# Kernel tuning notes

Hardware: AMD Instinct MI355X
Metric: run time of the kernel (lower is better)

The kernel has to match this reference:

```python
import jax, jax.numpy as jnp
import numpy as np

N, M, D = 8192, 8192, 256

def setup_inputs() -> dict:
    key = jax.random.key(0)
    k1, k2, k3, k4 = jax.random.split(key, 4)
    x1 = jax.random.normal(k1, (N, D), dtype=jnp.float32)
    x2 = jax.random.normal(k2, (M, D), dtype=jnp.float32)
    alpha_raw = jax.random.normal(k3, (D,), dtype=jnp.float32)      # nn.Parameter(torch.randn(input_dim))
    variance_raw = jnp.ones((1,), dtype=jnp.float32)                # nn.Parameter(torch.ones(1))
    return {"x1": x1, "x2": x2, "alpha_raw": alpha_raw, "variance_raw": variance_raw}

def reference(x1, x2, alpha_raw, variance_raw):
    # alpha = softmax(alpha_raw^2), variance = variance_raw^2
    alpha = jax.nn.softmax(alpha_raw ** 2)                          # (D,)
    variance = variance_raw ** 2                                    # (1,)
    # GEMM rewrite of sum_d alpha_d (x1_i - x2_j)^2:
    #   ||x1*sqrt(a)||^2 - 2 (x1*sqrt(a))(x2*sqrt(a))^T + ||x2*sqrt(a)||^2
    sa = jnp.sqrt(alpha)
    a = x1 * sa                                                     # (N, D)
    b = x2 * sa                                                     # (M, D)
    sq = (jnp.sum(a * a, axis=-1)[:, None]
          - 2.0 * (a @ b.T)
          + jnp.sum(b * b, axis=-1)[None, :])                       # (N, M)
    sq = jnp.maximum(sq, 0.0)  # numerical guard; exact value is non-negative
    kernel = variance * jnp.exp(-0.5 * sq)                          # (N, M)
    if kernel.shape[0] == 1:
        kernel = jnp.squeeze(kernel)
    return kernel
```

## Files before the change

### kernel.cpp

```cpp
#include <hip/hip_runtime.h>
#include <stdint.h>

#define NROWS 8192
#define MCOLS 8192
#define KDIM  256

typedef __bf16 bf16x8 __attribute__((ext_vector_type(8)));
typedef float  floatx4 __attribute__((ext_vector_type(4)));
typedef unsigned short ushort4v __attribute__((ext_vector_type(4)));

__device__ __forceinline__ unsigned short f32_to_bf16_rne(float f) {
    unsigned int u = __float_as_uint(f);
    u += 0x7FFFu + ((u >> 16) & 1u);
    return (unsigned short)(u >> 16);
}
__device__ __forceinline__ float bf16_to_f32(unsigned short h) {
    return __uint_as_float(((unsigned int)h) << 16);
}

__device__ __forceinline__ void async16(const void* g, void* l) {
    __builtin_amdgcn_global_load_lds(
        (const __attribute__((address_space(1))) unsigned int*)g,
        (__attribute__((address_space(3))) unsigned int*)l,
        16, 0, 0);
}

__global__ void prep_alpha(const float* __restrict__ araw, float* __restrict__ sa) {
    int d = threadIdx.x;
    float z = araw[d];
    z = z * z;
    float m = z;
#pragma unroll
    for (int off = 32; off; off >>= 1) m = fmaxf(m, __shfl_xor(m, off));
    __shared__ float wred[4];
    if ((d & 63) == 0) wred[d >> 6] = m;
    __syncthreads();
    float mx = fmaxf(fmaxf(wred[0], wred[1]), fmaxf(wred[2], wred[3]));
    float e = __expf(z - mx);
    float s = e;
#pragma unroll
    for (int off = 32; off; off >>= 1) s += __shfl_xor(s, off);
    __syncthreads();
    if ((d & 63) == 0) wred[d >> 6] = s;
    __syncthreads();
    float sum = wred[0] + wred[1] + wred[2] + wred[3];
    sa[d] = sqrtf(e / sum);
}

__global__ void prep_rows(const float* __restrict__ x1, const float* __restrict__ x2,
                          const float* __restrict__ sa,
                          unsigned short* __restrict__ Amat, unsigned short* __restrict__ Bmat,
                          float* __restrict__ ra, float* __restrict__ rb) {
    int wave = threadIdx.x >> 6;
    int lane = threadIdx.x & 63;
    int grow = blockIdx.x * 4 + wave;
    const float* x; unsigned short* mat; float* nrm; int row;
    if (grow < NROWS) { x = x1; mat = Amat; nrm = ra; row = grow; }
    else              { x = x2; mat = Bmat; nrm = rb; row = grow - NROWS; }

    floatx4 v  = *(const floatx4*)&x[(size_t)row * KDIM + lane * 4];
    floatx4 sv = *(const floatx4*)&sa[lane * 4];
    ushort4v h;
    float p = 0.0f;
#pragma unroll
    for (int j = 0; j < 4; ++j) {
        float f = v[j] * sv[j];
        unsigned short hh = f32_to_bf16_rne(f);
        h[j] = hh;
        float fv = bf16_to_f32(hh);
        p += fv * fv;
    }
    *(ushort4v*)&mat[(size_t)row * KDIM + lane * 4] = h;
#pragma unroll
    for (int off = 32; off; off >>= 1) p += __shfl_xor(p, off);
    if (lane == 0) nrm[row] = p;
}

__global__ __launch_bounds__(256) void rbf_gemm(
    const unsigned short* __restrict__ A, const unsigned short* __restrict__ B,
    const float* __restrict__ ra, const float* __restrict__ rb,
    const float* __restrict__ vraw, float* __restrict__ out)
{
    __shared__ unsigned short As[128 * 64];
    __shared__ unsigned short Bs[128 * 64];

    const int tid  = threadIdx.x;
    const int lane = tid & 63;
    const int wave = tid >> 6;

    const int g   = blockIdx.y * gridDim.x + blockIdx.x;
    const int xcd = g & 7;
    const int i   = g >> 3;
    const int bm  = (xcd >> 2) * 32 + (i >> 4);
    const int bn  = (xcd & 3) * 16 + (i & 15);

    const int wm = (wave & 1) * 64;
    const int wn = (wave >> 1) * 64;
    const int quad = lane >> 4;
    const int l15  = lane & 15;

    floatx4 acc[4][4];
#pragma unroll
    for (int tj = 0; tj < 4; tj++)
#pragma unroll
        for (int ti = 0; ti < 4; ti++) acc[tj][ti] = (floatx4)0.0f;

    for (int t = 0; t < 4; ++t) {
        int k0 = t * 64;
#pragma unroll
        for (int it = 0; it < 4; ++it) {
            int c   = it * 256 + tid;
            int row = c >> 3;
            int kc  = c & 7;
            int gkc = kc ^ (row & 7);
            const unsigned short* gA = A + (size_t)(bm * 128 + row) * KDIM + k0 + gkc * 8;
            const unsigned short* gB = B + (size_t)(bn * 128 + row) * KDIM + k0 + gkc * 8;
            async16(gA, &As[c * 8]);
            async16(gB, &Bs[c * 8]);
        }
        __syncthreads();

#pragma unroll
        for (int ks = 0; ks < 2; ++ks) {
            bf16x8 af[4], bfr[4];
            int kc = ks * 4 + quad;
#pragma unroll
            for (int tt = 0; tt < 4; ++tt) {
                int m   = wm + tt * 16 + l15;
                int sA  = m * 8 + (kc ^ (m & 7));
                af[tt]  = *(const bf16x8*)&As[sA * 8];
                int n   = wn + tt * 16 + l15;
                int sB  = n * 8 + (kc ^ (n & 7));
                bfr[tt] = *(const bf16x8*)&Bs[sB * 8];
            }
#pragma unroll
            for (int tj = 0; tj < 4; ++tj)
#pragma unroll
                for (int ti = 0; ti < 4; ++ti)
                    acc[tj][ti] = __builtin_amdgcn_mfma_f32_16x16x32_bf16(
                        bfr[tj], af[ti], acc[tj][ti], 0, 0, 0);
        }
        if (t < 3) __syncthreads();
    }

    float variance = vraw[0] * vraw[0];
#pragma unroll
    for (int ti = 0; ti < 4; ++ti) {
        int row = bm * 128 + wm + ti * 16 + l15;
        float rav = ra[row];
        float* orow = out + (size_t)row * MCOLS;
#pragma unroll
        for (int tj = 0; tj < 4; ++tj) {
            int nbase = bn * 128 + wn + tj * 16 + quad * 4;
            floatx4 rbv = *(const floatx4*)&rb[nbase];
            floatx4 val;
#pragma unroll
            for (int r = 0; r < 4; ++r) {
                float s = rav + rbv[r] - 2.0f * acc[tj][ti][r];
                s = fmaxf(s, 0.0f);
                val[r] = variance * __expf(-0.5f * s);
            }
            *(floatx4*)&orow[nbase] = val;
        }
    }
}

extern "C" void kernel_launch(void* const* d_in, const int* in_sizes, int n_in,
                              void* d_out, int out_size, void* d_ws, size_t ws_size,
                              hipStream_t stream) {
    const float* x1   = (const float*)d_in[0];
    const float* x2   = (const float*)d_in[1];
    const float* araw = (const float*)d_in[2];
    const float* vraw = (const float*)d_in[3];
    float* out = (float*)d_out;

    char* ws = (char*)d_ws;
    float* sa = (float*)ws;
    float* ra = (float*)(ws + 1024);
    float* rb = (float*)(ws + 1024 + 32768);
    unsigned short* Amat = (unsigned short*)(ws + 66560);
    unsigned short* Bmat = (unsigned short*)(ws + 66560 + (size_t)NROWS * KDIM * 2);

    prep_alpha<<<1, 256, 0, stream>>>(araw, sa);
    prep_rows<<<(NROWS + MCOLS) / 4, 256, 0, stream>>>(x1, x2, sa, Amat, Bmat, ra, rb);

    dim3 grid(MCOLS / 128, NROWS / 128);
    rbf_gemm<<<grid, 256, 0, stream>>>(Amat, Bmat, ra, rb, vraw, out);
}
```

Baseline: 304.6 us.

## Fuse alpha softmax into row prep and process two tiles per GEMM block

Each prep_rows block now computes the softmax of alpha itself into LDS, which removes the separate single-block prep_alpha launch and its global round trip. The GEMM kernel now launches 2048 blocks that each handle two output tiles. It issues the first k-slice load of the second tile before the first tile's epilogue so that load overlaps the exp/store work. Launch bounds request 4 blocks per CU. The trade-off is redundant softmax work in every prep block and fewer total blocks.

Result: slower. 339.5 us (+11.5%).

```diff
diff --git a/kernel.cpp b/kernel.cpp
--- a/kernel.cpp
+++ b/kernel.cpp
@@ -25,41 +25,41 @@
         16, 0, 0);
 }
 
-__global__ void prep_alpha(const float* __restrict__ araw, float* __restrict__ sa) {
-    int d = threadIdx.x;
-    float z = araw[d];
+__global__ void prep_rows(const float* __restrict__ x1, const float* __restrict__ x2,
+                          const float* __restrict__ araw,
+                          unsigned short* __restrict__ Amat, unsigned short* __restrict__ Bmat,
+                          float* __restrict__ ra, float* __restrict__ rb) {
+    __shared__ float sa_lds[256];
+    __shared__ float wred[8];
+    int tid  = threadIdx.x;
+    int wave = tid >> 6;
+    int lane = tid & 63;
+
+    float z = araw[tid];
     z = z * z;
     float m = z;
 #pragma unroll
     for (int off = 32; off; off >>= 1) m = fmaxf(m, __shfl_xor(m, off));
-    __shared__ float wred[4];
-    if ((d & 63) == 0) wred[d >> 6] = m;
+    if (lane == 0) wred[wave] = m;
     __syncthreads();
     float mx = fmaxf(fmaxf(wred[0], wred[1]), fmaxf(wred[2], wred[3]));
     float e = __expf(z - mx);
     float s = e;
 #pragma unroll
     for (int off = 32; off; off >>= 1) s += __shfl_xor(s, off);
+    if (lane == 0) wred[4 + wave] = s;
     __syncthreads();
-    if ((d & 63) == 0) wred[d >> 6] = s;
+    float sum = wred[4] + wred[5] + wred[6] + wred[7];
+    sa_lds[tid] = sqrtf(e / sum);
     __syncthreads();
-    float sum = wred[0] + wred[1] + wred[2] + wred[3];
-    sa[d] = sqrtf(e / sum);
-}
-
-__global__ void prep_rows(const float* __restrict__ x1, const float* __restrict__ x2,
-                          const float* __restrict__ sa,
-                          unsigned short* __restrict__ Amat, unsigned short* __restrict__ Bmat,
-                          float* __restrict__ ra, float* __restrict__ rb) {
-    int wave = threadIdx.x >> 6;
-    int lane = threadIdx.x & 63;
+
     int grow = blockIdx.x * 4 + wave;
     const float* x; unsigned short* mat; float* nrm; int row;
     if (grow < NROWS) { x = x1; mat = Amat; nrm = ra; row = grow; }
     else              { x = x2; mat = Bmat; nrm = rb; row = grow - NROWS; }
 
     floatx4 v  = *(const floatx4*)&x[(size_t)row * KDIM + lane * 4];
-    floatx4 sv = *(const floatx4*)&sa[lane * 4];
+    floatx4 sv = *(const floatx4*)&sa_lds[lane * 4];
     ushort4v h;
     float p = 0.0f;
 #pragma unroll
@@ -76,7 +76,7 @@
     if (lane == 0) nrm[row] = p;
 }
 
-__global__ __launch_bounds__(256) void rbf_gemm(
+__global__ __launch_bounds__(256, 4) void rbf_gemm(
     const unsigned short* __restrict__ A, const unsigned short* __restrict__ B,
     const float* __restrict__ ra, const float* __restrict__ rb,
     const float* __restrict__ vraw, float* __restrict__ out)
@@ -88,25 +88,22 @@
     const int lane = tid & 63;
     const int wave = tid >> 6;
 
-    const int g   = blockIdx.y * gridDim.x + blockIdx.x;
-    const int xcd = g & 7;
-    const int i   = g >> 3;
-    const int bm  = (xcd >> 2) * 32 + (i >> 4);
-    const int bn  = (xcd & 3) * 16 + (i & 15);
-
     const int wm = (wave & 1) * 64;
     const int wn = (wave >> 1) * 64;
     const int quad = lane >> 4;
     const int l15  = lane & 15;
 
-    floatx4 acc[4][4];
-#pragma unroll
-    for (int tj = 0; tj < 4; tj++)
-#pragma unroll
-        for (int ti = 0; ti < 4; ti++) acc[tj][ti] = (floatx4)0.0f;
-
-    for (int t = 0; t < 4; ++t) {
-        int k0 = t * 64;
+    int bmv[2], bnv[2];
+#pragma unroll
+    for (int tt = 0; tt < 2; ++tt) {
+        int g   = blockIdx.x + tt * 2048;
+        int xcd = g & 7;
+        int i   = g >> 3;
+        bmv[tt] = (xcd >> 2) * 32 + (i >> 4);
+        bnv[tt] = (xcd & 3) * 16 + (i & 15);
+    }
+
+    auto stage = [&](int bm, int bn, int k0) {
 #pragma unroll
         for (int it = 0; it < 4; ++it) {
             int c   = it * 256 + tid;
@@ -118,49 +115,71 @@
             async16(gA, &As[c * 8]);
             async16(gB, &Bs[c * 8]);
         }
-        __syncthreads();
-
-#pragma unroll
-        for (int ks = 0; ks < 2; ++ks) {
-            bf16x8 af[4], bfr[4];
-            int kc = ks * 4 + quad;
-#pragma unroll
-            for (int tt = 0; tt < 4; ++tt) {
-                int m   = wm + tt * 16 + l15;
-                int sA  = m * 8 + (kc ^ (m & 7));
-                af[tt]  = *(const bf16x8*)&As[sA * 8];
-                int n   = wn + tt * 16 + l15;
-                int sB  = n * 8 + (kc ^ (n & 7));
-                bfr[tt] = *(const bf16x8*)&Bs[sB * 8];
+    };
+
+    const float variance = vraw[0] * vraw[0];
+
+    stage(bmv[0], bnv[0], 0);
+
+#pragma unroll
+    for (int tt = 0; tt < 2; ++tt) {
+        const int bm = bmv[tt];
+        const int bn = bnv[tt];
+
+        floatx4 acc[4][4];
+#pragma unroll
+        for (int tj = 0; tj < 4; tj++)
+#pragma unroll
+            for (int ti = 0; ti < 4; ti++) acc[tj][ti] = (floatx4)0.0f;
+
+#pragma unroll
+        for (int t = 0; t < 4; ++t) {
+            __syncthreads();
+#pragma unroll
+            for (int ks = 0; ks < 2; ++ks) {
+                bf16x8 af[4], bfr[4];
+                int kc = ks * 4 + quad;
+#pragma unroll
+                for (int x = 0; x < 4; ++x) {
+                    int mm  = wm + x * 16 + l15;
+                    int sA  = mm * 8 + (kc ^ (mm & 7));
+                    af[x]   = *(const bf16x8*)&As[sA * 8];
+                    int nn  = wn + x * 16 + l15;
+                    int sB  = nn * 8 + (kc ^ (nn & 7));
+                    bfr[x]  = *(const bf16x8*)&Bs[sB * 8];
+                }
+#pragma unroll
+                for (int tj = 0; tj < 4; ++tj)
+#pragma unroll
+                    for (int ti = 0; ti < 4; ++ti)
+                        acc[tj][ti] = __builtin_amdgcn_mfma_f32_16x16x32_bf16(
+                            bfr[tj], af[ti], acc[tj][ti], 0, 0, 0);
             }
-#pragma unroll
-            for (int tj = 0; tj < 4; ++tj)
-#pragma unroll
-                for (int ti = 0; ti < 4; ++ti)
-                    acc[tj][ti] = __builtin_amdgcn_mfma_f32_16x16x32_bf16(
-                        bfr[tj], af[ti], acc[tj][ti], 0, 0, 0);
+            if (!(tt == 1 && t == 3)) {
+                __syncthreads();
+                if (t < 3)            stage(bm, bn, (t + 1) * 64);
+                else                  stage(bmv[1], bnv[1], 0);
+            }
         }
-        if (t < 3) __syncthreads();
-    }
-
-    float variance = vraw[0] * vraw[0];
-#pragma unroll
-    for (int ti = 0; ti < 4; ++ti) {
-        int row = bm * 128 + wm + ti * 16 + l15;
-        float rav = ra[row];
-        float* orow = out + (size_t)row * MCOLS;
-#pragma unroll
-        for (int tj = 0; tj < 4; ++tj) {
-            int nbase = bn * 128 + wn + tj * 16 + quad * 4;
-            floatx4 rbv = *(const floatx4*)&rb[nbase];
-            floatx4 val;
-#pragma unroll
-            for (int r = 0; r < 4; ++r) {
-                float s = rav + rbv[r] - 2.0f * acc[tj][ti][r];
-                s = fmaxf(s, 0.0f);
-                val[r] = variance * __expf(-0.5f * s);
+
+#pragma unroll
+        for (int ti = 0; ti < 4; ++ti) {
+            int row = bm * 128 + wm + ti * 16 + l15;
+            float rav = ra[row];
+            float* orow = out + (size_t)row * MCOLS;
+#pragma unroll
+            for (int tj = 0; tj < 4; ++tj) {
+                int nbase = bn * 128 + wn + tj * 16 + quad * 4;
+                floatx4 rbv = *(const floatx4*)&rb[nbase];
+                floatx4 val;
+#pragma unroll
+                for (int r = 0; r < 4; ++r) {
+                    float s = rav + rbv[r] - 2.0f * acc[tj][ti][r];
+                    s = fmaxf(s, 0.0f);
+                    val[r] = variance * __expf(-0.5f * s);
+                }
+                *(floatx4*)&orow[nbase] = val;
             }
-            *(floatx4*)&orow[nbase] = val;
         }
     }
 }
@@ -175,15 +194,12 @@
     float* out = (float*)d_out;
 
     char* ws = (char*)d_ws;
-    float* sa = (float*)ws;
     float* ra = (float*)(ws + 1024);
     float* rb = (float*)(ws + 1024 + 32768);
     unsigned short* Amat = (unsigned short*)(ws + 66560);
     unsigned short* Bmat = (unsigned short*)(ws + 66560 + (size_t)NROWS * KDIM * 2);
 
-    prep_alpha<<<1, 256, 0, stream>>>(araw, sa);
-    prep_rows<<<(NROWS + MCOLS) / 4, 256, 0, stream>>>(x1, x2, sa, Amat, Bmat, ra, rb);
-
-    dim3 grid(MCOLS / 128, NROWS / 128);
-    rbf_gemm<<<grid, 256, 0, stream>>>(Amat, Bmat, ra, rb, vraw, out);
-}
+    prep_rows<<<(NROWS + MCOLS) / 4, 256, 0, stream>>>(x1, x2, araw, Amat, Bmat, ra, rb);
+
+    rbf_gemm<<<2048, 256, 0, stream>>>(Amat, Bmat, ra, rb, vraw, out);
+}
```
